# Kernel tuning notes

Measured on AMD Instinct MI355X. Metric: run time of the kernel, lower is better.

The kernel has to match this reference:

```python
import jax, jax.numpy as jnp
import numpy as np

T, NE, NA, OBS, D, CH, VH, ITERS = 128, 64, 8, 64, 128, 128, 256, 2
B = NE * NA  # num_actors


def setup_inputs() -> dict:
    key = jax.random.key(0)
    ks = jax.random.split(key, 16)
    rn = lambda k, shape, s=0.05: jax.random.normal(k, shape, jnp.float32) * s
    z = lambda *shape: jnp.zeros(shape, jnp.float32)
    return dict(
        hidden=z(B, D),
        obs=rn(ks[0], (T, B, OBS), 1.0),
        dones=jax.random.bernoulli(ks[1], 0.05, (T, B)),
        embed1_w=rn(ks[2], (OBS, D)), embed1_b=z(D),
        embed2_w=rn(ks[3], (D, D)), embed2_b=z(D),
        gru_Wi=rn(ks[4], (D, 3 * D)), gru_bi=z(3 * D),
        gru_Wh=rn(ks[5], (D, 3 * D)), gru_bhn=z(D),
        couple_h_w=rn(ks[6], (2 * D, CH)), couple_h_b=z(CH),
        couple_out_w=rn(ks[7], (CH, 1)), couple_out_b=z(1),
        update_h_w=rn(ks[8], (2 * D, D)), update_h_b=z(D),
        update_out_w=rn(ks[9], (D, D)), update_out_b=z(D),
        value_h1_w=rn(ks[10], (D, VH)), value_h1_b=z(VH),
        value_h2_w=rn(ks[11], (VH, VH)), value_h2_b=z(VH),
        value_out_w=rn(ks[12], (VH, 1)), value_out_b=z(1),
    )


def _gru_scan(hidden, x, dones, Wi, bi, Wh, bhn):
    # flax GRUCell math: r,z gates (no hidden bias), n gate with hidden bias.
    def step(h, xd):
        xt, dt = xd
        h = jnp.where(dt[:, None], 0.0, h)  # reset carry on done
        gi = xt @ Wi + bi                   # [B, 3D]
        gh = h @ Wh                         # [B, 3D]
        i_r, i_z, i_n = jnp.split(gi, 3, axis=-1)
        h_r, h_z, h_n = jnp.split(gh, 3, axis=-1)
        r = jax.nn.sigmoid(i_r + h_r)
        zg = jax.nn.sigmoid(i_z + h_z)
        n = jnp.tanh(i_n + r * (h_n + bhn))
        new_h = (1.0 - zg) * n + zg * h
        return new_h, new_h
    return jax.lax.scan(step, hidden, (x, dones))


def reference(hidden, obs, dones,
              embed1_w, embed1_b, embed2_w, embed2_b,
              gru_Wi, gru_bi, gru_Wh, gru_bhn,
              couple_h_w, couple_h_b, couple_out_w, couple_out_b,
              update_h_w, update_h_b, update_out_w, update_out_b,
              value_h1_w, value_h1_b, value_h2_w, value_h2_b,
              value_out_w, value_out_b):
    # observation embedding MLP
    emb = jax.nn.relu(obs @ embed1_w + embed1_b)
    emb = jax.nn.relu(emb @ embed2_w + embed2_b)
    hidden, rnn_out = _gru_scan(hidden, emb, dones, gru_Wi, gru_bi, gru_Wh, gru_bhn)

    e = rnn_out.reshape(T, NE, NA, D)
    alive = (1.0 - dones.astype(jnp.float32)).reshape(T, NE, NA)
    e = e * alive[..., None]
    identity_mask = 1.0 - jnp.eye(NA, dtype=jnp.float32)

    # split-linear trick: couple_h(concat[h_i, h_j]) == h_i @ W1 + h_j @ W2 + b
    W1, W2 = couple_h_w[:D], couple_h_w[D:]
    U1, U2 = update_h_w[:D], update_h_w[D:]

    for _ in range(ITERS):
        a_i = jnp.einsum('teid,dh->teih', e, W1)  # [T,E,A,CH]
        a_j = jnp.einsum('tejd,dh->tejh', e, W2)
        Ch = jax.nn.relu(a_i[:, :, :, None, :] + a_j[:, :, None, :, :] + couple_h_b)  # [T,E,A,A,CH]
        C = jax.nn.sigmoid(jnp.einsum('teijh,h->teij', Ch, couple_out_w[:, 0]) + couple_out_b[0])
        C = C * alive[:, :, None, :] * identity_mask[None, None, :, :]
        context = jnp.einsum('teij,tejd->teid', C, e)
        delta = jax.nn.relu(e @ U1 + context @ U2 + update_h_b)
        delta = jax.nn.relu(delta @ update_out_w + update_out_b)
        e = (e + delta) * alive[..., None]

    v = jax.nn.relu(e @ value_h1_w + value_h1_b)
    v = jax.nn.relu(v @ value_h2_w + value_h2_b)
    v = (v @ value_out_w + value_out_b)[..., 0]  # [T,E,A]
    values = v.reshape(T, B)
    return hidden, values
```

## Files before the change

kernel.cpp:

```cpp
#include <hip/hip_runtime.h>
#include <hip/hip_bf16.h>
#include <math.h>

#define T_ 128
#define NE_ 64
#define NA_ 8
#define B_ 512
#define OBS_ 64
#define D_ 128
#define CH_ 128
#define VH_ 256
#define M_ (T_*B_)

typedef __attribute__((ext_vector_type(8))) short bf16x8;
typedef __attribute__((ext_vector_type(8))) _Float16 f16x8;
typedef __attribute__((ext_vector_type(4))) float f32x4;

__device__ __forceinline__ float sigmoidf_(float x){ return 1.f/(1.f+__expf(-x)); }
__device__ __forceinline__ unsigned short f2bu(float v){
  __hip_bfloat16 b = __float2bfloat16(v);
  return __builtin_bit_cast(unsigned short, b);
}
__device__ __forceinline__ float bu2f(unsigned short u){
  return __builtin_bit_cast(float, (unsigned int)u << 16);
}
__device__ __forceinline__ unsigned short f2hu(float v){
  _Float16 h = (_Float16)v;
  return __builtin_bit_cast(unsigned short, h);
}
__device__ __forceinline__ float hu2f(unsigned short u){
  return (float)__builtin_bit_cast(_Float16, u);
}

__global__ __launch_bounds__(256)
void embgi_k(const float* __restrict__ obs,
             const ushort* __restrict__ e1wT, const float* __restrict__ e1b,
             const ushort* __restrict__ e2wT, const float* __restrict__ e2b,
             const ushort* __restrict__ gWiT, const float* __restrict__ gbi,
             ushort* __restrict__ giH)
{
  __shared__ ushort S1[128*136];
  __shared__ ushort S2[128*136];
  const int tid  = threadIdx.x;
  const int lane = tid & 63, wave = tid >> 6;
  const int wm = wave >> 1, wn = wave & 1;
  const int quad = lane >> 4, ln = lane & 15;
  const int m0 = blockIdx.x * 128;

  f32x4 acc[4][4];

  #pragma unroll
  for (int i=0;i<8;i++){
    int c4 = tid + i*256;
    int m = c4 >> 4, kf = (c4 & 15) * 4;
    float4 v = *(const float4*)&obs[(size_t)(m0+m)*OBS_ + kf];
    ushort4 h; h.x=f2hu(v.x); h.y=f2hu(v.y); h.z=f2hu(v.z); h.w=f2hu(v.w);
    *(ushort4*)&S1[m*136 + kf] = h;
  }
  #pragma unroll
  for (int i=0;i<4;i++){
    int c8 = tid + i*256;
    int n = c8 >> 3, kq = (c8 & 7)*8;
    *(uint4*)&S2[n*136 + kq] = *(const uint4*)&e1wT[(size_t)n*64 + kq];
  }
  __syncthreads();

  #pragma unroll
  for (int i=0;i<4;i++)
    #pragma unroll
    for (int j=0;j<4;j++)
      #pragma unroll
      for (int r=0;r<4;r++) acc[i][j][r] = 0.f;
  #pragma unroll
  for (int ks=0; ks<2; ks++){
    const int kq = ks*32 + quad*8;
    f16x8 af[4], bfv[4];
    #pragma unroll
    for (int mt=0;mt<4;mt++)
      af[mt] = *(const f16x8*)&S1[(wm*64 + mt*16 + ln)*136 + kq];
    #pragma unroll
    for (int nt=0;nt<4;nt++)
      bfv[nt] = *(const f16x8*)&S2[(wn*64 + nt*16 + ln)*136 + kq];
    #pragma unroll
    for (int mt=0;mt<4;mt++)
      #pragma unroll
      for (int nt=0;nt<4;nt++)
        acc[mt][nt] = __builtin_amdgcn_mfma_f32_16x16x32_f16(af[mt], bfv[nt], acc[mt][nt], 0,0,0);
  }
  __syncthreads();

  #pragma unroll
  for (int mt=0;mt<4;mt++)
    #pragma unroll
    for (int r=0;r<4;r++){
      int rl = wm*64 + mt*16 + quad*4 + r;
      #pragma unroll
      for (int nt=0;nt<4;nt++){
        int cl = wn*64 + nt*16 + ln;
        S1[rl*136 + cl] = f2hu(fmaxf(acc[mt][nt][r] + e1b[cl], 0.f));
      }
    }
  #pragma unroll
  for (int i=0;i<8;i++){
    int c8 = tid + i*256;
    int n = c8 >> 4, kq = (c8 & 15)*8;
    *(uint4*)&S2[n*136 + kq] = *(const uint4*)&e2wT[(size_t)n*128 + kq];
  }
  __syncthreads();

  #pragma unroll
  for (int i=0;i<4;i++)
    #pragma unroll
    for (int j=0;j<4;j++)
      #pragma unroll
      for (int r=0;r<4;r++) acc[i][j][r] = 0.f;
  #pragma unroll
  for (int ks=0; ks<4; ks++){
    const int kq = ks*32 + quad*8;
    f16x8 af[4], bfv[4];
    #pragma unroll
    for (int mt=0;mt<4;mt++)
      af[mt] = *(const f16x8*)&S1[(wm*64 + mt*16 + ln)*136 + kq];
    #pragma unroll
    for (int nt=0;nt<4;nt++)
      bfv[nt] = *(const f16x8*)&S2[(wn*64 + nt*16 + ln)*136 + kq];
    #pragma unroll
    for (int mt=0;mt<4;mt++)
      #pragma unroll
      for (int nt=0;nt<4;nt++)
        acc[mt][nt] = __builtin_amdgcn_mfma_f32_16x16x32_f16(af[mt], bfv[nt], acc[mt][nt], 0,0,0);
  }
  __syncthreads();

  #pragma unroll
  for (int mt=0;mt<4;mt++)
    #pragma unroll
    for (int r=0;r<4;r++){
      int rl = wm*64 + mt*16 + quad*4 + r;
      #pragma unroll
      for (int nt=0;nt<4;nt++){
        int cl = wn*64 + nt*16 + ln;
        S1[rl*136 + cl] = f2hu(fmaxf(acc[mt][nt][r] + e2b[cl], 0.f));
      }
    }

  for (int c=0; c<3; c++){
    #pragma unroll
    for (int i=0;i<8;i++){
      int c8 = tid + i*256;
      int n = c8 >> 4, kq = (c8 & 15)*8;
      *(uint4*)&S2[n*136 + kq] = *(const uint4*)&gWiT[(size_t)(c*128+n)*128 + kq];
    }
    __syncthreads();
    #pragma unroll
    for (int i=0;i<4;i++)
      #pragma unroll
      for (int j=0;j<4;j++)
        #pragma unroll
        for (int r=0;r<4;r++) acc[i][j][r] = 0.f;
    #pragma unroll
    for (int ks=0; ks<4; ks++){
      const int kq = ks*32 + quad*8;
      f16x8 af[4], bfv[4];
      #pragma unroll
      for (int mt=0;mt<4;mt++)
        af[mt] = *(const f16x8*)&S1[(wm*64 + mt*16 + ln)*136 + kq];
      #pragma unroll
      for (int nt=0;nt<4;nt++)
        bfv[nt] = *(const f16x8*)&S2[(wn*64 + nt*16 + ln)*136 + kq];
      #pragma unroll
      for (int mt=0;mt<4;mt++)
        #pragma unroll
        for (int nt=0;nt<4;nt++)
          acc[mt][nt] = __builtin_amdgcn_mfma_f32_16x16x32_f16(af[mt], bfv[nt], acc[mt][nt], 0,0,0);
    }
    __syncthreads();
    #pragma unroll
    for (int mt=0;mt<4;mt++)
      #pragma unroll
      for (int r=0;r<4;r++){
        int row = m0 + wm*64 + mt*16 + quad*4 + r;
        #pragma unroll
        for (int nt=0;nt<4;nt++){
          int cl = wn*64 + nt*16 + ln;
          giH[(size_t)row*384 + c*128 + cl] = f2hu(acc[mt][nt][r] + gbi[c*128 + cl]);
        }
      }
  }
}

__global__ __launch_bounds__(256, 1)
void postgru_k(const __hip_bfloat16* __restrict__ Xe, const __hip_bfloat16* __restrict__ bcatT,
               const float* __restrict__ chb, const float* __restrict__ cow,
               const float* __restrict__ cob,
               const __hip_bfloat16* __restrict__ uhwT, const float* __restrict__ uhb,
               const __hip_bfloat16* __restrict__ uowT, const float* __restrict__ uob,
               const int* __restrict__ dones,
               const __hip_bfloat16* __restrict__ v1wT, const float* __restrict__ v1b,
               const __hip_bfloat16* __restrict__ v2wT, const float* __restrict__ v2b,
               const float* __restrict__ vow, const float* __restrict__ vob,
               float* __restrict__ values)
{
  __shared__ ushort S1[128*136];
  __shared__ ushort Bs[128*136];
  __shared__ alignas(16) ushort Pool[2*128*136];
  __shared__ alignas(16) float cbw[CH_], cww[CH_];
  __shared__ float Cs[4][NA_][NA_];
  const int tid  = threadIdx.x;
  const int lane = tid & 63, wave = tid >> 6;
  const int wm = wave >> 1, wn = wave & 1;
  const int quad = lane >> 4, ln = lane & 15;
  const int m0 = blockIdx.x * 128;

  ushort* XcS = Pool;
  float (*AI)[132] = (float(*)[132])(Pool + 128*136);
  float (*AJ)[132] = (float(*)[132])((char*)(Pool + 128*136) + 16896);

  #pragma unroll
  for (int i=0;i<8;i++){
    int c8 = tid + i*256;
    int m = c8 >> 4, kq = (c8 & 15)*8;
    *(uint4*)&S1[m*136 + kq] = *(const uint4*)((const ushort*)Xe + (size_t)(m0+m)*128 + kq);
  }
  if (tid < 128){ cbw[tid] = chb[tid]; cww[tid] = cow[tid]; }
  const float cob0 = cob[0];
  __syncthreads();

  for (int it=0; it<2; it++){
    for (int g=0; g<4; g++){
      const int r0 = g*32;
      #pragma unroll
      for (int i=0;i<8;i++){
        int c8 = tid + i*256;
        int n = c8 >> 4, kq = (c8 & 15)*8;
        *(uint4*)&Bs[n*136 + kq] = *(const uint4*)((const ushort*)bcatT + (size_t)n*128 + kq);
      }
      __syncthreads();
      {
        f32x4 acc[2][2];
        #pragma unroll
        for (int mt=0;mt<2;mt++)
          #pragma unroll
          for (int nt=0;nt<2;nt++)
            #pragma unroll
            for (int r=0;r<4;r++) acc[mt][nt][r] = 0.f;
        #pragma unroll
        for (int ks=0; ks<4; ks++){
          const int kq = ks*32 + quad*8;
          bf16x8 af[2], bfv[2];
          #pragma unroll
          for (int mt=0;mt<2;mt++)
            af[mt] = *(const bf16x8*)&S1[(r0 + mt*16 + ln)*136 + kq];
          #pragma unroll
          for (int nt=0;nt<2;nt++)
            bfv[nt] = *(const bf16x8*)&Bs[(wave*32 + nt*16 + ln)*136 + kq];
          #pragma unroll
          for (int mt=0;mt<2;mt++)
            #pragma unroll
            for (int nt=0;nt<2;nt++)
              acc[mt][nt] = __builtin_amdgcn_mfma_f32_16x16x32_bf16(af[mt], bfv[nt], acc[mt][nt], 0,0,0);
        }
        __syncthreads();
        #pragma unroll
        for (int mt=0;mt<2;mt++)
          #pragma unroll
          for (int r=0;r<4;r++)
            #pragma unroll
            for (int nt=0;nt<2;nt++)
              AI[mt*16 + quad*4 + r][wave*32 + nt*16 + ln] = acc[mt][nt][r];
      }
      #pragma unroll
      for (int i=0;i<8;i++){
        int c8 = tid + i*256;
        int n = c8 >> 4, kq = (c8 & 15)*8;
        *(uint4*)&Bs[n*136 + kq] = *(const uint4*)((const ushort*)bcatT + (size_t)(128+n)*128 + kq);
      }
      __syncthreads();
      {
        f32x4 acc[2][2];
        #pragma unroll
        for (int mt=0;mt<2;mt++)
          #pragma unroll
          for (int nt=0;nt<2;nt++)
            #pragma unroll
            for (int r=0;r<4;r++) acc[mt][nt][r] = 0.f;
        #pragma unroll
        for (int ks=0; ks<4; ks++){
          const int kq = ks*32 + quad*8;
          bf16x8 af[2], bfv[2];
          #pragma unroll
          for (int mt=0;mt<2;mt++)
            af[mt] = *(const bf16x8*)&S1[(r0 + mt*16 + ln)*136 + kq];
          #pragma unroll
          for (int nt=0;nt<2;nt++)
            bfv[nt] = *(const bf16x8*)&Bs[(wave*32 + nt*16 + ln)*136 + kq];
          #pragma unroll
          for (int mt=0;mt<2;mt++)
            #pragma unroll
            for (int nt=0;nt<2;nt++)
              acc[mt][nt] = __builtin_amdgcn_mfma_f32_16x16x32_bf16(af[mt], bfv[nt], acc[mt][nt], 0,0,0);
        }
        #pragma unroll
        for (int mt=0;mt<2;mt++)
          #pragma unroll
          for (int r=0;r<4;r++)
            #pragma unroll
            for (int nt=0;nt<2;nt++)
              AJ[mt*16 + quad*4 + r][wave*32 + nt*16 + ln] = acc[mt][nt][r];
      }
      __syncthreads();

      {
        const int env = tid >> 6;
        const int p = tid & 63, i = p >> 3, j = p & 7;
        const float* aiR = &AI[env*8 + i][0];
        const float* ajR = &AJ[env*8 + j][0];
        float s = 0.f;
        #pragma unroll
        for (int h4=0; h4<32; h4++){
          float4 a4 = *(const float4*)&aiR[h4*4];
          float4 b4 = *(const float4*)&ajR[h4*4];
          float4 c4 = *(const float4*)&cbw[h4*4];
          float4 w4 = *(const float4*)&cww[h4*4];
          s += fmaxf(a4.x + b4.x + c4.x, 0.f) * w4.x;
          s += fmaxf(a4.y + b4.y + c4.y, 0.f) * w4.y;
          s += fmaxf(a4.z + b4.z + c4.z, 0.f) * w4.z;
          s += fmaxf(a4.w + b4.w + c4.w, 0.f) * w4.w;
        }
        float Cv = sigmoidf_(s + cob0);
        Cs[env][i][j] = (i==j) ? 0.f : Cv;
      }
      __syncthreads();

      {
        const int lr = tid >> 3;
        const int env = lr >> 3, i = lr & 7;
        const int c0 = (tid & 7) * 16;
        #pragma unroll
        for (int cc=0; cc<4; cc++){
          int d = c0 + cc*4;
          float a0=0.f, a1=0.f, a2=0.f, a3=0.f;
          #pragma unroll
          for (int j=0;j<NA_;j++){
            float c = Cs[env][i][j];
            ushort4 e4 = *(const ushort4*)&S1[(r0 + env*8 + j)*136 + d];
            a0 = fmaf(c, bu2f(e4.x), a0);
            a1 = fmaf(c, bu2f(e4.y), a1);
            a2 = fmaf(c, bu2f(e4.z), a2);
            a3 = fmaf(c, bu2f(e4.w), a3);
          }
          ushort4 o; o.x=f2bu(a0); o.y=f2bu(a1); o.z=f2bu(a2); o.w=f2bu(a3);
          *(ushort4*)&XcS[(r0 + lr)*136 + d] = o;
        }
      }
      __syncthreads();
    }

    f32x4 acc[4][4];
    #pragma unroll
    for (int i=0;i<4;i++)
      #pragma unroll
      for (int j=0;j<4;j++)
        #pragma unroll
        for (int r=0;r<4;r++) acc[i][j][r] = 0.f;

    #pragma unroll
    for (int kc=0; kc<2; kc++){
      #pragma unroll
      for (int i=0;i<8;i++){
        int c8 = tid + i*256;
        int n = c8 >> 4, kq = (c8 & 15)*8;
        *(uint4*)&Bs[n*136 + kq] = *(const uint4*)((const ushort*)uhwT + (size_t)n*256 + kc*128 + kq);
      }
      __syncthreads();
      const ushort* Ab = kc ? XcS : S1;
      #pragma unroll
      for (int ks=0; ks<4; ks++){
        const int kq = ks*32 + quad*8;
        bf16x8 af[4], bfv[4];
        #pragma unroll
        for (int mt=0;mt<4;mt++)
          af[mt] = *(const bf16x8*)&Ab[(wm*64 + mt*16 + ln)*136 + kq];
        #pragma unroll
        for (int nt=0;nt<4;nt++)
          bfv[nt] = *(const bf16x8*)&Bs[(wn*64 + nt*16 + ln)*136 + kq];
        #pragma unroll
        for (int mt=0;mt<4;mt++)
          #pragma unroll
          for (int nt=0;nt<4;nt++)
            acc[mt][nt] = __builtin_amdgcn_mfma_f32_16x16x32_bf16(af[mt], bfv[nt], acc[mt][nt], 0,0,0);
      }
      __syncthreads();
    }

    #pragma unroll
    for (int i=0;i<8;i++){
      int c8 = tid + i*256;
      int n = c8 >> 4, kq = (c8 & 15)*8;
      *(uint4*)&Bs[n*136 + kq] = *(const uint4*)((const ushort*)uowT + (size_t)n*128 + kq);
    }
    #pragma unroll
    for (int mt=0;mt<4;mt++)
      #pragma unroll
      for (int r=0;r<4;r++){
        int rl = wm*64 + mt*16 + quad*4 + r;
        #pragma unroll
        for (int nt=0;nt<4;nt++){
          int cl = wn*64 + nt*16 + ln;
          XcS[rl*136 + cl] = f2bu(fmaxf(acc[mt][nt][r] + uhb[cl], 0.f));
        }
      }
    __syncthreads();

    f32x4 acc2[4][4];
    #pragma unroll
    for (int i=0;i<4;i++)
      #pragma unroll
      for (int j=0;j<4;j++)
        #pragma unroll
        for (int r=0;r<4;r++) acc2[i][j][r] = 0.f;
    #pragma unroll
    for (int ks=0; ks<4; ks++){
      const int kq = ks*32 + quad*8;
      bf16x8 af[4], bfv[4];
      #pragma unroll
      for (int mt=0;mt<4;mt++)
        af[mt] = *(const bf16x8*)&XcS[(wm*64 + mt*16 + ln)*136 + kq];
      #pragma unroll
      for (int nt=0;nt<4;nt++)
        bfv[nt] = *(const bf16x8*)&Bs[(wn*64 + nt*16 + ln)*136 + kq];
      #pragma unroll
      for (int mt=0;mt<4;mt++)
        #pragma unroll
        for (int nt=0;nt<4;nt++)
          acc2[mt][nt] = __builtin_amdgcn_mfma_f32_16x16x32_bf16(af[mt], bfv[nt], acc2[mt][nt], 0,0,0);
    }
    #pragma unroll
    for (int mt=0;mt<4;mt++){
      #pragma unroll
      for (int r=0;r<4;r++){
        int rl = wm*64 + mt*16 + quad*4 + r;
        int row = m0 + rl;
        float al = (dones[row]!=0) ? 0.f : 1.f;
        #pragma unroll
        for (int nt=0;nt<4;nt++){
          int cl = wn*64 + nt*16 + ln;
          float v = fmaxf(acc2[mt][nt][r] + uob[cl], 0.f);
          v += bu2f(S1[rl*136 + cl]);
          v *= al;
          S1[rl*136 + cl] = f2bu(v);
        }
      }
    }
    __syncthreads();
  }

  ushort* V1 = Pool;

  for (int h=0; h<2; h++){
    #pragma unroll
    for (int i=0;i<8;i++){
      int c8 = tid + i*256;
      int n = c8 >> 4, kq = (c8 & 15)*8;
      *(uint4*)&Bs[n*136 + kq] = *(const uint4*)((const ushort*)v1wT + (size_t)(h*128+n)*128 + kq);
    }
    __syncthreads();
    f32x4 acc[4][4];
    #pragma unroll
    for (int i=0;i<4;i++)
      #pragma unroll
      for (int j=0;j<4;j++)
        #pragma unroll
        for (int r=0;r<4;r++) acc[i][j][r] = 0.f;
    #pragma unroll
    for (int ks=0; ks<4; ks++){
      const int kq = ks*32 + quad*8;
      bf16x8 af[4], bfv[4];
      #pragma unroll
      for (int mt=0;mt<4;mt++)
        af[mt] = *(const bf16x8*)&S1[(wm*64 + mt*16 + ln)*136 + kq];
      #pragma unroll
      for (int nt=0;nt<4;nt++)
        bfv[nt] = *(const bf16x8*)&Bs[(wn*64 + nt*16 + ln)*136 + kq];
      #pragma unroll
      for (int mt=0;mt<4;mt++)
        #pragma unroll
        for (int nt=0;nt<4;nt++)
          acc[mt][nt] = __builtin_amdgcn_mfma_f32_16x16x32_bf16(af[mt], bfv[nt], acc[mt][nt], 0,0,0);
    }
    __syncthreads();
    #pragma unroll
    for (int mt=0;mt<4;mt++)
      #pragma unroll
      for (int r=0;r<4;r++){
        int rl = wm*64 + mt*16 + quad*4 + r;
        #pragma unroll
        for (int nt=0;nt<4;nt++){
          int cl = wn*64 + nt*16 + ln;
          V1[h*128*136 + rl*136 + cl] = f2bu(fmaxf(acc[mt][nt][r] + v1b[h*128 + cl], 0.f));
        }
      }
  }

  float s[4][4];
  #pragma unroll
  for (int mt=0;mt<4;mt++)
    #pragma unroll
    for (int r=0;r<4;r++) s[mt][r] = 0.f;

  for (int oc=0; oc<2; oc++){
    f32x4 acc[4][4];
    #pragma unroll
    for (int i=0;i<4;i++)
      #pragma unroll
      for (int j=0;j<4;j++)
        #pragma unroll
        for (int r=0;r<4;r++) acc[i][j][r] = 0.f;
    for (int kh=0; kh<2; kh++){
      #pragma unroll
      for (int i=0;i<8;i++){
        int c8 = tid + i*256;
        int n = c8 >> 4, kq = (c8 & 15)*8;
        *(uint4*)&Bs[n*136 + kq] = *(const uint4*)((const ushort*)v2wT + (size_t)(oc*128+n)*256 + kh*128 + kq);
      }
      __syncthreads();
      #pragma unroll
      for (int ks=0; ks<4; ks++){
        const int kq = ks*32 + quad*8;
        bf16x8 af[4], bfv[4];
        #pragma unroll
        for (int mt=0;mt<4;mt++)
          af[mt] = *(const bf16x8*)&V1[kh*128*136 + (wm*64 + mt*16 + ln)*136 + kq];
        #pragma unroll
        for (int nt=0;nt<4;nt++)
          bfv[nt] = *(const bf16x8*)&Bs[(wn*64 + nt*16 + ln)*136 + kq];
        #pragma unroll
        for (int mt=0;mt<4;mt++)
          #pragma unroll
          for (int nt=0;nt<4;nt++)
            acc[mt][nt] = __builtin_amdgcn_mfma_f32_16x16x32_bf16(af[mt], bfv[nt], acc[mt][nt], 0,0,0);
      }
      __syncthreads();
    }
    float v2bv[4], voww[4];
    #pragma unroll
    for (int nt=0;nt<4;nt++){
      int col = oc*128 + wn*64 + nt*16 + ln;
      v2bv[nt] = v2b[col];
      voww[nt] = vow[col];
    }
    #pragma unroll
    for (int mt=0;mt<4;mt++)
      #pragma unroll
      for (int r=0;r<4;r++){
        float p = 0.f;
        #pragma unroll
        for (int nt=0;nt<4;nt++)
          p += fmaxf(acc[mt][nt][r] + v2bv[nt], 0.f) * voww[nt];
        s[mt][r] += p;
      }
  }

  #pragma unroll
  for (int off=1; off<16; off<<=1)
    #pragma unroll
    for (int mt=0;mt<4;mt++)
      #pragma unroll
      for (int r=0;r<4;r++)
        s[mt][r] += __shfl_xor(s[mt][r], off);
  if (ln == 0){
    float add = (wn == 0) ? vob[0] : 0.f;
    #pragma unroll
    for (int mt=0;mt<4;mt++)
      #pragma unroll
      for (int r=0;r<4;r++)
        atomicAdd(&values[m0 + wm*64 + mt*16 + quad*4 + r], s[mt][r] + add);
  }
}

__global__ __launch_bounds__(512, 1)
void grum8_k(const ushort* __restrict__ gih, const float* __restrict__ hidden0,
             const int* __restrict__ dones, const float* __restrict__ gWh,
             const float* __restrict__ bhn, __hip_bfloat16* __restrict__ eb_out,
             float* __restrict__ hout)
{
  __shared__ ushort wstg[32*392];
  __shared__ ushort hb[2][16*136];
  __shared__ float  dnS[T_*4];
  const int tid  = threadIdx.x;
  const int lane = tid & 63, wave = tid >> 6;
  const int quad = lane >> 4, ln = lane & 15;
  const int r0   = blockIdx.x * 4;
  const int col  = wave*16 + ln;
  const int lnb  = ln & 12;

  dnS[tid] = (dones[(size_t)(tid>>2)*B_ + r0 + (tid&3)] != 0) ? 1.f : 0.f;
  const float bhnr = bhn[col];

  for (int i=tid; i<16*136; i+=512){ hb[0][i]=0; hb[1][i]=0; }

  f16x8 bf[3][4];
  #pragma unroll
  for (int kc=0; kc<4; kc++){
    for (int i=tid; i<32*384; i+=512){
      int kk = i/384, c = i - kk*384;
      wstg[kk*392 + c] = f2hu(gWh[(size_t)(kc*32+kk)*384 + c]);
    }
    __syncthreads();
    #pragma unroll
    for (int g=0; g<3; g++){
      int c = g*128 + col;
      ushort tmp[8];
      #pragma unroll
      for (int j=0;j<8;j++) tmp[j] = wstg[(quad*8+j)*392 + c];
      bf[g][kc] = *(const f16x8*)tmp;
    }
    __syncthreads();
  }

  float hc = hidden0[(size_t)(r0+quad)*D_ + col];
  if (dnS[quad] > 0.5f) hc = 0.f;
  hb[0][(quad*4)*136 + col] = f2hu(hc);
  __syncthreads();

  const ushort* gbase = gih + ((size_t)(r0+quad))*384;
  const size_t  gstep = (size_t)B_*384;

  float c_r, c_z, c_n;
  c_r = hu2f(gbase[col]); c_z = hu2f(gbase[col+128]); c_n = hu2f(gbase[col+256]);
  ushort aR,aZ,aN, bR,bZ,bN, cR,cZ,cN, dR,dZ,dN;
  { const ushort* gp = gbase + 1*gstep; aR = gp[col]; aZ = gp[col+128]; aN = gp[col+256]; }
  { const ushort* gp = gbase + 2*gstep; bR = gp[col]; bZ = gp[col+128]; bN = gp[col+256]; }
  { const ushort* gp = gbase + 3*gstep; cR = gp[col]; cZ = gp[col+128]; cN = gp[col+256]; }
  dR=0; dZ=0; dN=0;

  ushort pend_eu = 0;

#define GSTEP(t, IR,IZ,IN, OR,OZ,ON)                                          \
  {                                                                           \
    if ((t) > 0)                                                              \
      ((ushort*)eb_out)[((size_t)((t)-1)*B_ + r0+quad)*D_ + col] = pend_eu;   \
    { int tl = (t)+4; if (tl > T_-1) tl = T_-1;                               \
      const ushort* gp = gbase + (size_t)tl*gstep;                            \
      OR = gp[col]; OZ = gp[col+128]; ON = gp[col+256]; }                     \
    const ushort* hbuf = hb[(t)&1];                                           \
    f32x4 accA[3], accB[3];                                                   \
    _Pragma("unroll")                                                         \
    for (int g=0;g<3;g++){                                                    \
      _Pragma("unroll")                                                       \
      for (int r=0;r<4;r++){ accA[g][r]=0.f; accB[g][r]=0.f; }                \
    }                                                                         \
    _Pragma("unroll")                                                         \
    for (int ks=0; ks<2; ks++){                                               \
      f16x8 ahA = *(const f16x8*)&hbuf[lnb*136 + (2*ks  )*32 + quad*8];       \
      f16x8 ahB = *(const f16x8*)&hbuf[lnb*136 + (2*ks+1)*32 + quad*8];       \
      _Pragma("unroll")                                                       \
      for (int g=0;g<3;g++){                                                  \
        accA[g] = __builtin_amdgcn_mfma_f32_16x16x32_f16(ahA, bf[g][2*ks  ], accA[g], 0,0,0); \
        accB[g] = __builtin_amdgcn_mfma_f32_16x16x32_f16(ahB, bf[g][2*ks+1], accB[g], 0,0,0); \
      }                                                                       \
    }                                                                         \
    const float dnow  = dnS[(t)*4 + quad];                                    \
    const float dnext = ((t)+1 < T_) ? dnS[((t)+1)*4 + quad] : 0.f;           \
    float rg = sigmoidf_(c_r + accA[0][0] + accB[0][0]);                      \
    float zg = sigmoidf_(c_z + accA[1][0] + accB[1][0]);                      \
    float x  = c_n + rg*(accA[2][0] + accB[2][0] + bhnr);                     \
    float ng = 2.f/(1.f+__expf(-2.f*x)) - 1.f;                                \
    float hnew = (1.f - zg)*ng + zg*hc;                                       \
    pend_eu = f2bu(hnew*(1.f-dnow));                                          \
    float hv = (dnext > 0.5f) ? 0.f : hnew;                                   \
    hc = hv;                                                                  \
    hb[((t)+1)&1][(quad*4)*136 + col] = f2hu(hv);                             \
    asm volatile("s_waitcnt lgkmcnt(0)\n\ts_barrier" ::: "memory");           \
    c_r = hu2f(IR); c_z = hu2f(IZ); c_n = hu2f(IN);                           \
  }

  for (int t=0; t<T_; t+=4){
    GSTEP(t+0, aR,aZ,aN, dR,dZ,dN);
    GSTEP(t+1, bR,bZ,bN, aR,aZ,aN);
    GSTEP(t+2, cR,cZ,cN, bR,bZ,bN);
    GSTEP(t+3, dR,dZ,dN, cR,cZ,cN);
  }
#undef GSTEP

  ((ushort*)eb_out)[((size_t)(T_-1)*B_ + r0+quad)*D_ + col] = pend_eu;
  hout[(size_t)(r0+quad)*D_ + col] = hc;
}

__global__ __launch_bounds__(256)
void packall_k(const float* __restrict__ e1w, ushort* __restrict__ e1T,
               const float* __restrict__ e2w, ushort* __restrict__ e2T,
               const float* __restrict__ gWi, ushort* __restrict__ giT,
               const float* __restrict__ chw, __hip_bfloat16* __restrict__ bcatT,
               const float* __restrict__ uhw, __hip_bfloat16* __restrict__ uhwT,
               const float* __restrict__ uow, __hip_bfloat16* __restrict__ uowT,
               const float* __restrict__ v1w, __hip_bfloat16* __restrict__ v1wT,
               const float* __restrict__ v2w, __hip_bfloat16* __restrict__ v2wT)
{
  const int b = blockIdx.x, tid = threadIdx.x;
  if (b < 32){
    int idx = b*256 + tid;
    int n = idx >> 6, k = idx & 63;
    e1T[idx] = f2hu(e1w[k*128 + n]);
  } else if (b < 96){
    int idx = (b-32)*256 + tid;
    int n = idx >> 7, k = idx & 127;
    e2T[idx] = f2hu(e2w[k*128 + n]);
  } else if (b < 288){
    int idx = (b-96)*256 + tid;
    int n = idx >> 7, k = idx & 127;
    giT[idx] = f2hu(gWi[k*384 + n]);
  } else if (b < 416){
    int idx = (b-288)*256 + tid;
    int n = idx >> 7, k = idx & 127;
    float v = (n < 128) ? chw[k*128 + n] : chw[(128+k)*128 + (n-128)];
    bcatT[idx] = __float2bfloat16(v);
  } else if (b < 544){
    int idx = (b-416)*256 + tid;
    int r = idx >> 7, c = idx & 127;
    uhwT[c*256 + r] = __float2bfloat16(uhw[idx]);
  } else if (b < 608){
    int idx = (b-544)*256 + tid;
    int r = idx >> 7, c = idx & 127;
    uowT[c*128 + r] = __float2bfloat16(uow[idx]);
  } else if (b < 736){
    int idx = (b-608)*256 + tid;
    int r = idx >> 8, c = idx & 255;
    v1wT[c*128 + r] = __float2bfloat16(v1w[idx]);
  } else {
    int idx = (b-736)*256 + tid;
    int r = idx >> 8, c = idx & 255;
    v2wT[c*256 + r] = __float2bfloat16(v2w[idx]);
  }
}

extern "C" void kernel_launch(void* const* d_in, const int* in_sizes, int n_in,
                              void* d_out, int out_size, void* d_ws, size_t ws_size,
                              hipStream_t stream) {
  const float* hidden = (const float*)d_in[0];
  const float* obs    = (const float*)d_in[1];
  const int*   dones  = (const int*)  d_in[2];
  const float* e1w = (const float*)d_in[3];
  const float* e1b = (const float*)d_in[4];
  const float* e2w = (const float*)d_in[5];
  const float* e2b = (const float*)d_in[6];
  const float* gWi = (const float*)d_in[7];
  const float* gbi = (const float*)d_in[8];
  const float* gWh = (const float*)d_in[9];
  const float* gbhn= (const float*)d_in[10];
  const float* chw = (const float*)d_in[11];
  const float* chb = (const float*)d_in[12];
  const float* cow = (const float*)d_in[13];
  const float* cob = (const float*)d_in[14];
  const float* uhw = (const float*)d_in[15];
  const float* uhb = (const float*)d_in[16];
  const float* uow = (const float*)d_in[17];
  const float* uob = (const float*)d_in[18];
  const float* v1w = (const float*)d_in[19];
  const float* v1b = (const float*)d_in[20];
  const float* v2w = (const float*)d_in[21];
  const float* v2b = (const float*)d_in[22];
  const float* vow = (const float*)d_in[23];
  const float* vob = (const float*)d_in[24];
  (void)in_sizes; (void)n_in; (void)out_size;

  float* out_hidden = (float*)d_out;
  float* out_values = (float*)d_out + (size_t)B_*D_;

  float* ws = (float*)d_ws;
  ushort* giH   = (ushort*)(ws + 10485760);
  __hip_bfloat16* Xe = (__hip_bfloat16*)(ws + 23068672);
  ushort* wb    = (ushort*)(ws + 27262976);
  if (ws_size < (size_t)27500000 * sizeof(float)) return;

  __hip_bfloat16* bcatT = (__hip_bfloat16*)wb;
  __hip_bfloat16* uhwT  = (__hip_bfloat16*)wb + 32768;
  __hip_bfloat16* uowT  = (__hip_bfloat16*)wb + 65536;
  __hip_bfloat16* v1wT  = (__hip_bfloat16*)wb + 81920;
  __hip_bfloat16* v2wT  = (__hip_bfloat16*)wb + 114688;
  ushort* e1wT = wb + 180224;
  ushort* e2wT = wb + 188416;
  ushort* gWiT = wb + 204800;

  dim3 blk(256);
  hipMemsetAsync(out_values, 0, (size_t)M_*sizeof(float), stream);
  packall_k<<<dim3(992), blk, 0, stream>>>(
    e1w, e1wT, e2w, e2wT, gWi, gWiT,
    chw, bcatT, uhw, uhwT, uow, uowT, v1w, v1wT, v2w, v2wT);

  embgi_k<<<dim3(512), blk, 0, stream>>>(obs, e1wT, e1b, e2wT, e2b, gWiT, gbi, giH);

  grum8_k<<<dim3(128), dim3(512), 0, stream>>>(giH, hidden, dones, gWh, gbhn, Xe, out_hidden);

  postgru_k<<<dim3(512), blk, 0, stream>>>(Xe, bcatT, chb, cow, cob,
                                           uhwT, uhb, uowT, uob, dones,
                                           v1wT, v1b, v2wT, v2b, vow, vob, out_values);
}
```

Before: 362.3 us.

## Double postgru block to 512 threads and replace atomics with shared reduction

```diff
diff --git a/kernel.cpp b/kernel.cpp
--- a/kernel.cpp
+++ b/kernel.cpp
@@ -189,7 +189,7 @@
   }
 }
 
-__global__ __launch_bounds__(256, 1)
+__global__ __launch_bounds__(512, 1)
 void postgru_k(const __hip_bfloat16* __restrict__ Xe, const __hip_bfloat16* __restrict__ bcatT,
                const float* __restrict__ chb, const float* __restrict__ cow,
                const float* __restrict__ cob,
@@ -206,6 +206,7 @@
   __shared__ alignas(16) ushort Pool[2*128*136];
   __shared__ alignas(16) float cbw[CH_], cww[CH_];
   __shared__ float Cs[4][NA_][NA_];
+  __shared__ float SRed[128];
   const int tid  = threadIdx.x;
   const int lane = tid & 63, wave = tid >> 6;
   const int wm = wave >> 1, wn = wave & 1;
@@ -217,8 +218,8 @@
   float (*AJ)[132] = (float(*)[132])((char*)(Pool + 128*136) + 16896);
 
   #pragma unroll
-  for (int i=0;i<8;i++){
-    int c8 = tid + i*256;
+  for (int i=0;i<4;i++){
+    int c8 = tid + i*512;
     int m = c8 >> 4, kq = (c8 & 15)*8;
     *(uint4*)&S1[m*136 + kq] = *(const uint4*)((const ushort*)Xe + (size_t)(m0+m)*128 + kq);
   }
@@ -229,120 +230,126 @@
   for (int it=0; it<2; it++){
     for (int g=0; g<4; g++){
       const int r0 = g*32;
-      #pragma unroll
-      for (int i=0;i<8;i++){
-        int c8 = tid + i*256;
+      const int wrow = wave >> 2;
+      const int wcol = wave & 3;
+
+      #pragma unroll
+      for (int i=0;i<4;i++){
+        int c8 = tid + i*512;
         int n = c8 >> 4, kq = (c8 & 15)*8;
         *(uint4*)&Bs[n*136 + kq] = *(const uint4*)((const ushort*)bcatT + (size_t)n*128 + kq);
       }
       __syncthreads();
       {
-        f32x4 acc[2][2];
-        #pragma unroll
-        for (int mt=0;mt<2;mt++)
+        f32x4 accc[2];
+        #pragma unroll
+        for (int nt=0;nt<2;nt++)
           #pragma unroll
-          for (int nt=0;nt<2;nt++)
-            #pragma unroll
-            for (int r=0;r<4;r++) acc[mt][nt][r] = 0.f;
+          for (int r=0;r<4;r++) accc[nt][r] = 0.f;
         #pragma unroll
         for (int ks=0; ks<4; ks++){
           const int kq = ks*32 + quad*8;
-          bf16x8 af[2], bfv[2];
+          bf16x8 af = *(const bf16x8*)&S1[(r0 + wrow*16 + ln)*136 + kq];
           #pragma unroll
-          for (int mt=0;mt<2;mt++)
-            af[mt] = *(const bf16x8*)&S1[(r0 + mt*16 + ln)*136 + kq];
-          #pragma unroll
-          for (int nt=0;nt<2;nt++)
-            bfv[nt] = *(const bf16x8*)&Bs[(wave*32 + nt*16 + ln)*136 + kq];
-          #pragma unroll
-          for (int mt=0;mt<2;mt++)
-            #pragma unroll
-            for (int nt=0;nt<2;nt++)
-              acc[mt][nt] = __builtin_amdgcn_mfma_f32_16x16x32_bf16(af[mt], bfv[nt], acc[mt][nt], 0,0,0);
+          for (int nt=0;nt<2;nt++){
+            bf16x8 bfv = *(const bf16x8*)&Bs[(wcol*32 + nt*16 + ln)*136 + kq];
+            accc[nt] = __builtin_amdgcn_mfma_f32_16x16x32_bf16(af, bfv, accc[nt], 0,0,0);
+          }
         }
         __syncthreads();
         #pragma unroll
-        for (int mt=0;mt<2;mt++)
+        for (int nt=0;nt<2;nt++)
           #pragma unroll
           for (int r=0;r<4;r++)
-            #pragma unroll
-            for (int nt=0;nt<2;nt++)
-              AI[mt*16 + quad*4 + r][wave*32 + nt*16 + ln] = acc[mt][nt][r];
-      }
-      #pragma unroll
-      for (int i=0;i<8;i++){
-        int c8 = tid + i*256;
+            AI[wrow*16 + quad*4 + r][wcol*32 + nt*16 + ln] = accc[nt][r];
+      }
+      #pragma unroll
+      for (int i=0;i<4;i++){
+        int c8 = tid + i*512;
         int n = c8 >> 4, kq = (c8 & 15)*8;
         *(uint4*)&Bs[n*136 + kq] = *(const uint4*)((const ushort*)bcatT + (size_t)(128+n)*128 + kq);
       }
       __syncthreads();
       {
-        f32x4 acc[2][2];
-        #pragma unroll
-        for (int mt=0;mt<2;mt++)
+        f32x4 accc[2];
+        #pragma unroll
+        for (int nt=0;nt<2;nt++)
           #pragma unroll
-          for (int nt=0;nt<2;nt++)
-            #pragma unroll
-            for (int r=0;r<4;r++) acc[mt][nt][r] = 0.f;
+          for (int r=0;r<4;r++) accc[nt][r] = 0.f;
         #pragma unroll
         for (int ks=0; ks<4; ks++){
           const int kq = ks*32 + quad*8;
-          bf16x8 af[2], bfv[2];
+          bf16x8 af = *(const bf16x8*)&S1[(r0 + wrow*16 + ln)*136 + kq];
           #pragma unroll
-          for (int mt=0;mt<2;mt++)
-            af[mt] = *(const bf16x8*)&S1[(r0 + mt*16 + ln)*136 + kq];
-          #pragma unroll
-          for (int nt=0;nt<2;nt++)
-            bfv[nt] = *(const bf16x8*)&Bs[(wave*32 + nt*16 + ln)*136 + kq];
-          #pragma unroll
-          for (int mt=0;mt<2;mt++)
-            #pragma unroll
-            for (int nt=0;nt<2;nt++)
-              acc[mt][nt] = __builtin_amdgcn_mfma_f32_16x16x32_bf16(af[mt], bfv[nt], acc[mt][nt], 0,0,0);
+          for (int nt=0;nt<2;nt++){
+            bf16x8 bfv = *(const bf16x8*)&Bs[(wcol*32 + nt*16 + ln)*136 + kq];
+            accc[nt] = __builtin_amdgcn_mfma_f32_16x16x32_bf16(af, bfv, accc[nt], 0,0,0);
+          }
         }
         #pragma unroll
-        for (int mt=0;mt<2;mt++)
+        for (int nt=0;nt<2;nt++)
           #pragma unroll
           for (int r=0;r<4;r++)
-            #pragma unroll
-            for (int nt=0;nt<2;nt++)
-              AJ[mt*16 + quad*4 + r][wave*32 + nt*16 + ln] = acc[mt][nt][r];
+            AJ[wrow*16 + quad*4 + r][wcol*32 + nt*16 + ln] = accc[nt][r];
       }
       __syncthreads();
 
       {
-        const int env = tid >> 6;
-        const int p = tid & 63, i = p >> 3, j = p & 7;
+        const int env = tid >> 7;
+        const int i   = (tid >> 4) & 7;
+        const int jg  = (tid >> 3) & 1;
+        const int hq  = tid & 7;
         const float* aiR = &AI[env*8 + i][0];
-        const float* ajR = &AJ[env*8 + j][0];
-        float s = 0.f;
-        #pragma unroll
-        for (int h4=0; h4<32; h4++){
-          float4 a4 = *(const float4*)&aiR[h4*4];
-          float4 b4 = *(const float4*)&ajR[h4*4];
-          float4 c4 = *(const float4*)&cbw[h4*4];
-          float4 w4 = *(const float4*)&cww[h4*4];
-          s += fmaxf(a4.x + b4.x + c4.x, 0.f) * w4.x;
-          s += fmaxf(a4.y + b4.y + c4.y, 0.f) * w4.y;
-          s += fmaxf(a4.z + b4.z + c4.z, 0.f) * w4.z;
-          s += fmaxf(a4.w + b4.w + c4.w, 0.f) * w4.w;
+        const float* aj0 = &AJ[env*8 + jg*4 + 0][0];
+        const float* aj1 = &AJ[env*8 + jg*4 + 1][0];
+        const float* aj2 = &AJ[env*8 + jg*4 + 2][0];
+        const float* aj3 = &AJ[env*8 + jg*4 + 3][0];
+        float s0=0.f, s1=0.f, s2=0.f, s3=0.f;
+        #pragma unroll
+        for (int t=0; t<4; t++){
+          int h = (hq + t*8)*4;
+          float4 a4 = *(const float4*)&aiR[h];
+          float4 c4 = *(const float4*)&cbw[h];
+          float4 w4 = *(const float4*)&cww[h];
+          float px = a4.x + c4.x, py = a4.y + c4.y, pz = a4.z + c4.z, pw = a4.w + c4.w;
+          float4 b0 = *(const float4*)&aj0[h];
+          s0 += fmaxf(px+b0.x,0.f)*w4.x + fmaxf(py+b0.y,0.f)*w4.y
+              + fmaxf(pz+b0.z,0.f)*w4.z + fmaxf(pw+b0.w,0.f)*w4.w;
+          float4 b1 = *(const float4*)&aj1[h];
+          s1 += fmaxf(px+b1.x,0.f)*w4.x + fmaxf(py+b1.y,0.f)*w4.y
+              + fmaxf(pz+b1.z,0.f)*w4.z + fmaxf(pw+b1.w,0.f)*w4.w;
+          float4 b2 = *(const float4*)&aj2[h];
+          s2 += fmaxf(px+b2.x,0.f)*w4.x + fmaxf(py+b2.y,0.f)*w4.y
+              + fmaxf(pz+b2.z,0.f)*w4.z + fmaxf(pw+b2.w,0.f)*w4.w;
+          float4 b3 = *(const float4*)&aj3[h];
+          s3 += fmaxf(px+b3.x,0.f)*w4.x + fmaxf(py+b3.y,0.f)*w4.y
+              + fmaxf(pz+b3.z,0.f)*w4.z + fmaxf(pw+b3.w,0.f)*w4.w;
         }
-        float Cv = sigmoidf_(s + cob0);
-        Cs[env][i][j] = (i==j) ? 0.f : Cv;
+        s0 += __shfl_xor(s0,1); s0 += __shfl_xor(s0,2); s0 += __shfl_xor(s0,4);
+        s1 += __shfl_xor(s1,1); s1 += __shfl_xor(s1,2); s1 += __shfl_xor(s1,4);
+        s2 += __shfl_xor(s2,1); s2 += __shfl_xor(s2,2); s2 += __shfl_xor(s2,4);
+        s3 += __shfl_xor(s3,1); s3 += __shfl_xor(s3,2); s3 += __shfl_xor(s3,4);
+        if (hq == 0){
+          int j0 = jg*4;
+          float c0 = sigmoidf_(s0 + cob0); Cs[env][i][j0+0] = (i==j0+0)?0.f:c0;
+          float c1 = sigmoidf_(s1 + cob0); Cs[env][i][j0+1] = (i==j0+1)?0.f:c1;
+          float c2 = sigmoidf_(s2 + cob0); Cs[env][i][j0+2] = (i==j0+2)?0.f:c2;
+          float c3 = sigmoidf_(s3 + cob0); Cs[env][i][j0+3] = (i==j0+3)?0.f:c3;
+        }
       }
       __syncthreads();
 
       {
-        const int lr = tid >> 3;
-        const int env = lr >> 3, i = lr & 7;
-        const int c0 = (tid & 7) * 16;
-        #pragma unroll
-        for (int cc=0; cc<4; cc++){
+        const int lr = tid >> 4;
+        const int env = lr >> 3, ii = lr & 7;
+        const int c0 = (tid & 15) * 8;
+        #pragma unroll
+        for (int cc=0; cc<2; cc++){
           int d = c0 + cc*4;
           float a0=0.f, a1=0.f, a2=0.f, a3=0.f;
           #pragma unroll
           for (int j=0;j<NA_;j++){
-            float c = Cs[env][i][j];
+            float c = Cs[env][ii][j];
             ushort4 e4 = *(const ushort4*)&S1[(r0 + env*8 + j)*136 + d];
             a0 = fmaf(c, bu2f(e4.x), a0);
             a1 = fmaf(c, bu2f(e4.y), a1);
@@ -356,9 +363,9 @@
       __syncthreads();
     }
 
-    f32x4 acc[4][4];
-    #pragma unroll
-    for (int i=0;i<4;i++)
+    f32x4 acc[2][4];
+    #pragma unroll
+    for (int i=0;i<2;i++)
       #pragma unroll
       for (int j=0;j<4;j++)
         #pragma unroll
@@ -367,8 +374,8 @@
     #pragma unroll
     for (int kc=0; kc<2; kc++){
       #pragma unroll
-      for (int i=0;i<8;i++){
-        int c8 = tid + i*256;
+      for (int i=0;i<4;i++){
+        int c8 = tid + i*512;
         int n = c8 >> 4, kq = (c8 & 15)*8;
         *(uint4*)&Bs[n*136 + kq] = *(const uint4*)((const ushort*)uhwT + (size_t)n*256 + kc*128 + kq);
       }
@@ -377,15 +384,15 @@
       #pragma unroll
       for (int ks=0; ks<4; ks++){
         const int kq = ks*32 + quad*8;
-        bf16x8 af[4], bfv[4];
-        #pragma unroll
-        for (int mt=0;mt<4;mt++)
-          af[mt] = *(const bf16x8*)&Ab[(wm*64 + mt*16 + ln)*136 + kq];
+        bf16x8 af[2], bfv[4];
+        #pragma unroll
+        for (int mt=0;mt<2;mt++)
+          af[mt] = *(const bf16x8*)&Ab[(wm*32 + mt*16 + ln)*136 + kq];
         #pragma unroll
         for (int nt=0;nt<4;nt++)
           bfv[nt] = *(const bf16x8*)&Bs[(wn*64 + nt*16 + ln)*136 + kq];
         #pragma unroll
-        for (int mt=0;mt<4;mt++)
+        for (int mt=0;mt<2;mt++)
           #pragma unroll
           for (int nt=0;nt<4;nt++)
             acc[mt][nt] = __builtin_amdgcn_mfma_f32_16x16x32_bf16(af[mt], bfv[nt], acc[mt][nt], 0,0,0);
@@ -394,16 +401,16 @@
     }
 
     #pragma unroll
-    for (int i=0;i<8;i++){
-      int c8 = tid + i*256;
+    for (int i=0;i<4;i++){
+      int c8 = tid + i*512;
       int n = c8 >> 4, kq = (c8 & 15)*8;
       *(uint4*)&Bs[n*136 + kq] = *(const uint4*)((const ushort*)uowT + (size_t)n*128 + kq);
     }
     #pragma unroll
-    for (int mt=0;mt<4;mt++)
+    for (int mt=0;mt<2;mt++)
       #pragma unroll
       for (int r=0;r<4;r++){
-        int rl = wm*64 + mt*16 + quad*4 + r;
+        int rl = wm*32 + mt*16 + quad*4 + r;
         #pragma unroll
         for (int nt=0;nt<4;nt++){
           int cl = wn*64 + nt*16 + ln;
@@ -412,9 +419,9 @@
       }
     __syncthreads();
 
-    f32x4 acc2[4][4];
-    #pragma unroll
-    for (int i=0;i<4;i++)
+    f32x4 acc2[2][4];
+    #pragma unroll
+    for (int i=0;i<2;i++)
       #pragma unroll
       for (int j=0;j<4;j++)
         #pragma unroll
@@ -422,24 +429,24 @@
     #pragma unroll
     for (int ks=0; ks<4; ks++){
       const int kq = ks*32 + quad*8;
-      bf16x8 af[4], bfv[4];
-      #pragma unroll
-      for (int mt=0;mt<4;mt++)
-        af[mt] = *(const bf16x8*)&XcS[(wm*64 + mt*16 + ln)*136 + kq];
+      bf16x8 af[2], bfv[4];
+      #pragma unroll
+      for (int mt=0;mt<2;mt++)
+        af[mt] = *(const bf16x8*)&XcS[(wm*32 + mt*16 + ln)*136 + kq];
       #pragma unroll
       for (int nt=0;nt<4;nt++)
         bfv[nt] = *(const bf16x8*)&Bs[(wn*64 + nt*16 + ln)*136 + kq];
       #pragma unroll
-      for (int mt=0;mt<4;mt++)
+      for (int mt=0;mt<2;mt++)
         #pragma unroll
         for (int nt=0;nt<4;nt++)
           acc2[mt][nt] = __builtin_amdgcn_mfma_f32_16x16x32_bf16(af[mt], bfv[nt], acc2[mt][nt], 0,0,0);
     }
     #pragma unroll
-    for (int mt=0;mt<4;mt++){
+    for (int mt=0;mt<2;mt++){
       #pragma unroll
       for (int r=0;r<4;r++){
-        int rl = wm*64 + mt*16 + quad*4 + r;
+        int rl = wm*32 + mt*16 + quad*4 + r;
         int row = m0 + rl;
         float al = (dones[row]!=0) ? 0.f : 1.f;
         #pragma unroll
@@ -459,15 +466,15 @@
 
   for (int h=0; h<2; h++){
     #pragma unroll
-    for (int i=0;i<8;i++){
-      int c8 = tid + i*256;
+    for (int i=0;i<4;i++){
+      int c8 = tid + i*512;
       int n = c8 >> 4, kq = (c8 & 15)*8;
       *(uint4*)&Bs[n*136 + kq] = *(const uint4*)((const ushort*)v1wT + (size_t)(h*128+n)*128 + kq);
     }
     __syncthreads();
-    f32x4 acc[4][4];
-    #pragma unroll
-    for (int i=0;i<4;i++)
+    f32x4 acc[2][4];
+    #pragma unroll
+    for (int i=0;i<2;i++)
       #pragma unroll
       for (int j=0;j<4;j++)
         #pragma unroll
@@ -475,25 +482,25 @@
     #pragma unroll
     for (int ks=0; ks<4; ks++){
       const int kq = ks*32 + quad*8;
-      bf16x8 af[4], bfv[4];
-      #pragma unroll
-      for (int mt=0;mt<4;mt++)
-        af[mt] = *(const bf16x8*)&S1[(wm*64 + mt*16 + ln)*136 + kq];
+      bf16x8 af[2], bfv[4];
+      #pragma unroll
+      for (int mt=0;mt<2;mt++)
+        af[mt] = *(const bf16x8*)&S1[(wm*32 + mt*16 + ln)*136 + kq];
       #pragma unroll
       for (int nt=0;nt<4;nt++)
         bfv[nt] = *(const bf16x8*)&Bs[(wn*64 + nt*16 + ln)*136 + kq];
       #pragma unroll
-      for (int mt=0;mt<4;mt++)
+      for (int mt=0;mt<2;mt++)
         #pragma unroll
         for (int nt=0;nt<4;nt++)
           acc[mt][nt] = __builtin_amdgcn_mfma_f32_16x16x32_bf16(af[mt], bfv[nt], acc[mt][nt], 0,0,0);
     }
     __syncthreads();
     #pragma unroll
-    for (int mt=0;mt<4;mt++)
+    for (int mt=0;mt<2;mt++)
       #pragma unroll
       for (int r=0;r<4;r++){
-        int rl = wm*64 + mt*16 + quad*4 + r;
+        int rl = wm*32 + mt*16 + quad*4 + r;
         #pragma unroll
         for (int nt=0;nt<4;nt++){
           int cl = wn*64 + nt*16 + ln;
@@ -502,24 +509,24 @@
       }
   }
 
-  float s[4][4];
-  #pragma unroll
-  for (int mt=0;mt<4;mt++)
+  float s[2][4];
+  #pragma unroll
+  for (int mt=0;mt<2;mt++)
     #pragma unroll
     for (int r=0;r<4;r++) s[mt][r] = 0.f;
 
   for (int oc=0; oc<2; oc++){
-    f32x4 acc[4][4];
-    #pragma unroll
-    for (int i=0;i<4;i++)
+    f32x4 acc[2][4];
+    #pragma unroll
+    for (int i=0;i<2;i++)
       #pragma unroll
       for (int j=0;j<4;j++)
         #pragma unroll
         for (int r=0;r<4;r++) acc[i][j][r] = 0.f;
     for (int kh=0; kh<2; kh++){
       #pragma unroll
-      for (int i=0;i<8;i++){
-        int c8 = tid + i*256;
+      for (int i=0;i<4;i++){
+        int c8 = tid + i*512;
         int n = c8 >> 4, kq = (c8 & 15)*8;
         *(uint4*)&Bs[n*136 + kq] = *(const uint4*)((const ushort*)v2wT + (size_t)(oc*128+n)*256 + kh*128 + kq);
       }
@@ -527,15 +534,15 @@
       #pragma unroll
       for (int ks=0; ks<4; ks++){
         const int kq = ks*32 + quad*8;
-        bf16x8 af[4], bfv[4];
-        #pragma unroll
-        for (int mt=0;mt<4;mt++)
-          af[mt] = *(const bf16x8*)&V1[kh*128*136 + (wm*64 + mt*16 + ln)*136 + kq];
+        bf16x8 af[2], bfv[4];
+        #pragma unroll
+        for (int mt=0;mt<2;mt++)
+          af[mt] = *(const bf16x8*)&V1[kh*128*136 + (wm*32 + mt*16 + ln)*136 + kq];
         #pragma unroll
         for (int nt=0;nt<4;nt++)
           bfv[nt] = *(const bf16x8*)&Bs[(wn*64 + nt*16 + ln)*136 + kq];
         #pragma unroll
-        for (int mt=0;mt<4;mt++)
+        for (int mt=0;mt<2;mt++)
           #pragma unroll
           for (int nt=0;nt<4;nt++)
             acc[mt][nt] = __builtin_amdgcn_mfma_f32_16x16x32_bf16(af[mt], bfv[nt], acc[mt][nt], 0,0,0);
@@ -550,7 +557,7 @@
       voww[nt] = vow[col];
     }
     #pragma unroll
-    for (int mt=0;mt<4;mt++)
+    for (int mt=0;mt<2;mt++)
       #pragma unroll
       for (int r=0;r<4;r++){
         float p = 0.f;
@@ -564,17 +571,27 @@
   #pragma unroll
   for (int off=1; off<16; off<<=1)
     #pragma unroll
-    for (int mt=0;mt<4;mt++)
+    for (int mt=0;mt<2;mt++)
       #pragma unroll
       for (int r=0;r<4;r++)
         s[mt][r] += __shfl_xor(s[mt][r], off);
-  if (ln == 0){
-    float add = (wn == 0) ? vob[0] : 0.f;
-    #pragma unroll
-    for (int mt=0;mt<4;mt++)
+  if (ln == 0 && wn == 1){
+    #pragma unroll
+    for (int mt=0;mt<2;mt++)
       #pragma unroll
       for (int r=0;r<4;r++)
-        atomicAdd(&values[m0 + wm*64 + mt*16 + quad*4 + r], s[mt][r] + add);
+        SRed[wm*32 + mt*16 + quad*4 + r] = s[mt][r];
+  }
+  __syncthreads();
+  if (ln == 0 && wn == 0){
+    float vob0 = vob[0];
+    #pragma unroll
+    for (int mt=0;mt<2;mt++)
+      #pragma unroll
+      for (int r=0;r<4;r++){
+        int rl = wm*32 + mt*16 + quad*4 + r;
+        values[m0 + rl] = s[mt][r] + SRed[rl] + vob0;
+      }
   }
 }
 
@@ -783,7 +800,6 @@
   ushort* gWiT = wb + 204800;
 
   dim3 blk(256);
-  hipMemsetAsync(out_values, 0, (size_t)M_*sizeof(float), stream);
   packall_k<<<dim3(992), blk, 0, stream>>>(
     e1w, e1wT, e2w, e2wT, gWi, gWiT,
     chw, bcatT, uhw, uhwT, uow, uowT, v1w, v1wT, v2w, v2wT);
@@ -792,7 +808,7 @@
 
   grum8_k<<<dim3(128), dim3(512), 0, stream>>>(giH, hidden, dones, gWh, gbhn, Xe, out_hidden);
 
-  postgru_k<<<dim3(512), blk, 0, stream>>>(Xe, bcatT, chb, cow, cob,
-                                           uhwT, uhb, uowT, uob, dones,
-                                           v1wT, v1b, v2wT, v2b, vow, vob, out_values);
+  postgru_k<<<dim3(512), dim3(512), 0, stream>>>(Xe, bcatT, chb, cow, cob,
+                                                 uhwT, uhb, uowT, uob, dones,
+                                                 v1wT, v1b, v2wT, v2b, vow, vob, out_values);
 }
```

Result: faster. 309.8 us (-14.5%).
